# Optimization experiments

Hardware: AMD Instinct MI355X
Metric: run time of the kernel (lower is better)

Reference implementation:

```python
import jax, jax.numpy as jnp
import numpy as np

N = 300000
H = 700
W_GRID = 700
CIN = 64
COUT = 64
K = 9


def setup_inputs() -> dict:
    rng = np.random.default_rng(0)
    lin = rng.permutation(H * W_GRID)[:N]
    ys = (lin // W_GRID).astype(np.int64)
    xs = (lin % W_GRID).astype(np.int64)
    grid = np.full(H * W_GRID, -1, np.int32)
    grid[lin] = np.arange(N, dtype=np.int32)
    offs = [(dy, dx) for dy in (-1, 0, 1) for dx in (-1, 0, 1)]

    def build(d):
        nbr = np.full((K, N), -1, np.int32)
        for k, (dy, dx) in enumerate(offs):
            ny = ys + dy * d
            nx = xs + dx * d
            valid = (ny >= 0) & (ny < H) & (nx >= 0) & (nx < W_GRID)
            l = np.clip(ny * W_GRID + nx, 0, H * W_GRID - 1)
            nbr[k] = np.where(valid, grid[l], -1)
        return jnp.asarray(nbr)

    nbr_d1 = build(1)
    nbr_d2 = build(2)

    key = jax.random.key(0)
    ks = jax.random.split(key, 16)
    f32 = jnp.float32

    def bn(k, c):
        s = jax.random.uniform(k, (c,), f32, 0.5, 1.5)
        b = jax.random.normal(jax.random.fold_in(k, 1), (c,), f32) * 0.1
        return s, b

    features = jax.random.normal(ks[0], (N, CIN), f32)
    W1 = jax.random.normal(ks[1], (K, CIN, COUT), f32) * 0.05
    W2a = jax.random.normal(ks[2], (CIN, COUT // 2), f32) * 0.05
    W2b = jax.random.normal(ks[3], (K, COUT // 2, COUT), f32) * 0.05
    W3 = jax.random.normal(ks[4], (K, CIN, COUT), f32) * 0.05
    Wf = jax.random.normal(ks[5], (3 * COUT, COUT), f32) * 0.05
    A1_w = jax.random.normal(ks[6], (3 * COUT, COUT // 4), f32) * 0.1
    A1_b = jnp.zeros((COUT // 4,), f32)
    A2_w = jax.random.normal(ks[7], (COUT // 4, 3 * COUT), f32) * 0.1
    A2_b = jnp.zeros((3 * COUT,), f32)
    bn1_s, bn1_b = bn(ks[8], COUT)
    bn2a_s, bn2a_b = bn(ks[9], COUT // 2)
    bn2b_s, bn2b_b = bn(ks[10], COUT)
    bn3_s, bn3_b = bn(ks[11], COUT)
    bnf_s, bnf_b = bn(ks[12], COUT)

    return dict(features=features, W1=W1, bn1_s=bn1_s, bn1_b=bn1_b,
                W2a=W2a, bn2a_s=bn2a_s, bn2a_b=bn2a_b,
                W2b=W2b, bn2b_s=bn2b_s, bn2b_b=bn2b_b,
                W3=W3, bn3_s=bn3_s, bn3_b=bn3_b,
                A1_w=A1_w, A1_b=A1_b, A2_w=A2_w, A2_b=A2_b,
                Wf=Wf, bnf_s=bnf_s, bnf_b=bnf_b,
                nbr_d1=nbr_d1, nbr_d2=nbr_d2)


def _sconv(f, nbr, W):
    # f: [N, Cin], nbr: [K, N] (-1 = no neighbor), W: [K, Cin, Cout]
    mask = (nbr >= 0)[..., None]                      # [K, N, 1]
    g = jnp.where(mask, f[jnp.clip(nbr, 0)], 0.0)     # [K, N, Cin] gather
    return jnp.einsum('knc,kcd->nd', g, W)            # [N, Cout]


def _bnrelu(x, s, b):
    # inference-mode BatchNorm folded into affine scale/shift, then ReLU
    return jax.nn.relu(x * s + b)


def reference(features, W1, bn1_s, bn1_b, W2a, bn2a_s, bn2a_b, W2b, bn2b_s, bn2b_b,
              W3, bn3_s, bn3_b, A1_w, A1_b, A2_w, A2_b, Wf, bnf_s, bnf_b,
              nbr_d1, nbr_d2):
    # path 1: 3x3 sparse conv + BN + ReLU
    feat1 = _bnrelu(_sconv(features, nbr_d1, W1), bn1_s, bn1_b)
    # path 2: 1x1 bottleneck + 3x3 sparse conv
    h = _bnrelu(features @ W2a, bn2a_s, bn2a_b)
    feat2 = _bnrelu(_sconv(h, nbr_d1, W2b), bn2b_s, bn2b_b)
    # path 3: 3x3 dilated (d=2) sparse conv
    feat3 = _bnrelu(_sconv(features, nbr_d2, W3), bn3_s, bn3_b)
    ms = jnp.concatenate([feat1, feat2, feat3], axis=1)   # [N, 3*Cout]
    # SE-style attention from global max pool over active sites
    pooled = jnp.max(ms, axis=0)                          # [3*Cout]
    attn = jax.nn.sigmoid(jax.nn.relu(pooled @ A1_w + A1_b) @ A2_w + A2_b)
    ms = ms * attn
    # 1x1 fusion conv + BN + ReLU
    fused = _bnrelu(ms @ Wf, bnf_s, bnf_b)                # [N, Cout]
    return fused
```

## Files before the change

kernel.cpp:

```cpp
#include <hip/hip_runtime.h>

#define N_PTS 300000
#define NPAD  300032
#define ZROW  N_PTS

typedef _Float16 f16;
typedef _Float16 f16x8 __attribute__((ext_vector_type(8)));
typedef float    f32x4 __attribute__((ext_vector_type(4)));

__device__ __forceinline__ f16 f2h(float x) { return (f16)x; }

union u4f16 { uint4 u; f16x8 h; };

#define HEAD_BLOCKS (NPAD / 256)
#define WP_BLOCKS   361


__global__ __launch_bounds__(256) void k_head(
    const float* __restrict__ feat, const float* __restrict__ W2a,
    const float* __restrict__ s2a, const float* __restrict__ b2a,
    const float* __restrict__ W1, const float* __restrict__ W2b,
    const float* __restrict__ W3,
    f16* __restrict__ featf, f16* __restrict__ hf,
    f16* __restrict__ Wt1, f16* __restrict__ Wt2b, f16* __restrict__ Wt3,
    float* __restrict__ pooled)
{
    if (blockIdx.x >= HEAD_BLOCKS) {
        int i = (blockIdx.x - HEAD_BLOCKS) * 256 + threadIdx.x;
        if (i < 36864) {
            int j = i & 7, lane = (i >> 3) & 63, nt = (i >> 9) & 3,
                ks = (i >> 11) & 1, k = i >> 12;
            int d = ks * 32 + (lane >> 4) * 8 + j, c = nt * 16 + (lane & 15);
            Wt1[i] = f2h(W1[(k << 12) + (d << 6) + c]);
        } else if (i < 73728) {
            int ii = i - 36864;
            int j = ii & 7, lane = (ii >> 3) & 63, nt = (ii >> 9) & 3,
                ks = (ii >> 11) & 1, k = ii >> 12;
            int d = ks * 32 + (lane >> 4) * 8 + j, c = nt * 16 + (lane & 15);
            Wt3[ii] = f2h(W3[(k << 12) + (d << 6) + c]);
        } else if (i < 92160) {
            int ii = i - 73728;
            int j = ii & 7, lane = (ii >> 3) & 63, nt = (ii >> 9) & 3, k = ii >> 11;
            int d = (lane >> 4) * 8 + j, c = nt * 16 + (lane & 15);
            Wt2b[ii] = f2h(W2b[k * 2048 + (d << 6) + c]);
        } else if (i < 92352) {
            pooled[i - 92160] = 0.f;
        }
        return;
    }

    int lane = threadIdx.x & 63, wave = threadIdx.x >> 6;
    int n0 = (blockIdx.x * 4 + wave) * 64;
    int ln = lane & 15, q = lane >> 4;

    f16x8 a[4][2];
#pragma unroll
    for (int mt = 0; mt < 4; mt++) {
        int n = n0 + mt * 16 + ln;
#pragma unroll
        for (int ks = 0; ks < 2; ks++) {
            u4f16 v;
            if (n < N_PTS) {
                const float* p = feat + (long)n * 64 + ks * 32 + q * 8;
                float4 lo = *(const float4*)p;
                float4 hi = *(const float4*)(p + 4);
                v.h[0] = f2h(lo.x); v.h[1] = f2h(lo.y);
                v.h[2] = f2h(lo.z); v.h[3] = f2h(lo.w);
                v.h[4] = f2h(hi.x); v.h[5] = f2h(hi.y);
                v.h[6] = f2h(hi.z); v.h[7] = f2h(hi.w);
            } else {
                v.u = make_uint4(0u, 0u, 0u, 0u);
            }
            a[mt][ks] = v.h;
            *(uint4*)(featf + (long)n * 64 + ks * 32 + q * 8) = v.u;
        }
    }

    f32x4 acc[4][2];
    for (int mt = 0; mt < 4; mt++) for (int nt = 0; nt < 2; nt++)
        acc[mt][nt] = (f32x4){0.f, 0.f, 0.f, 0.f};
#pragma unroll
    for (int ks = 0; ks < 2; ks++)
#pragma unroll
        for (int nt = 0; nt < 2; nt++) {
            f16x8 b;
#pragma unroll
            for (int j = 0; j < 8; j++)
                b[j] = f2h(W2a[(ks * 32 + q * 8 + j) * 32 + nt * 16 + ln]);
#pragma unroll
            for (int mt = 0; mt < 4; mt++)
                acc[mt][nt] = __builtin_amdgcn_mfma_f32_16x16x32_f16(a[mt][ks], b, acc[mt][nt], 0, 0, 0);
        }

#pragma unroll
    for (int nt = 0; nt < 2; nt++) {
        int ch = nt * 16 + ln;
        float s = s2a[ch], bb = b2a[ch];
#pragma unroll
        for (int mt = 0; mt < 4; mt++)
#pragma unroll
            for (int r = 0; r < 4; r++) {
                int n = n0 + mt * 16 + q * 4 + r;
                float v = (n < N_PTS) ? fmaxf(acc[mt][nt][r] * s + bb, 0.f) : 0.f;
                hf[(long)n * 32 + ch] = f2h(v);
            }
    }
}

template <int CIN>
__device__ __forceinline__ void loadrows(
    uint4 (&dst)[4][CIN / 32], const int (&idx)[4],
    const f16* __restrict__ src, int q)
{
#pragma unroll
    for (int mt = 0; mt < 4; mt++) {
        const f16* p = src + (long)idx[mt] * CIN + q * 8;
#pragma unroll
        for (int ks = 0; ks < CIN / 32; ks++)
            dst[mt][ks] = *(const uint4*)(p + ks * 32);
    }
}

__device__ __forceinline__ void loadidx(
    int (&dst)[4], const int* __restrict__ nbr, int k, int n0, int ln)
{
    const int* nb = nbr + k * N_PTS;
#pragma unroll
    for (int mt = 0; mt < 4; mt++) {
        int nn = n0 + mt * 16 + ln;
        int v = (nn < N_PTS) ? nb[nn] : -1;
        dst[mt] = (v < 0) ? ZROW : v;
    }
}

template <int CIN>
__device__ __forceinline__ void conv_path(
    const f16* __restrict__ src, const f16* WtL,
    const int* __restrict__ nbr,
    int lane, int n0,
    const float* __restrict__ bns, const float* __restrict__ bnb,
    f16* __restrict__ msf, int colBase, float* __restrict__ pooled)
{
    constexpr int KS = CIN / 32;
    int ln = lane & 15, q = lane >> 4;

    f32x4 acc[4][4];
    for (int mt = 0; mt < 4; mt++) for (int nt = 0; nt < 4; nt++)
        acc[mt][nt] = (f32x4){0.f, 0.f, 0.f, 0.f};

    int  idxr[4][4];
    uint4 raw[4][4][KS];

#pragma unroll
    for (int k = 0; k < 4; k++) loadidx(idxr[k], nbr, k, n0, ln);
#pragma unroll
    for (int k = 0; k < 3; k++) loadrows<CIN>(raw[k], idxr[k], src, q);
    __builtin_amdgcn_sched_barrier(0);

#pragma unroll
    for (int k = 0; k < 9; k++) {
        if (k + 3 < 9) loadrows<CIN>(raw[(k + 3) & 3], idxr[(k + 3) & 3], src, q);
        if (k + 4 < 9) loadidx(idxr[k & 3], nbr, k + 4, n0, ln);
        __builtin_amdgcn_sched_barrier(0);
        const f16* Wk = WtL + k * (KS * 4 * 512);
        __builtin_amdgcn_s_setprio(1);
#pragma unroll
        for (int ks = 0; ks < KS; ks++)
#pragma unroll
            for (int nt = 0; nt < 4; nt++) {
                f16x8 b = *(const f16x8*)(Wk + (ks * 4 + nt) * 512 + lane * 8);
#pragma unroll
                for (int mt = 0; mt < 4; mt++) {
                    u4f16 v; v.u = raw[k & 3][mt][ks];
                    acc[mt][nt] = __builtin_amdgcn_mfma_f32_16x16x32_f16(v.h, b, acc[mt][nt], 0, 0, 0);
                }
            }
        __builtin_amdgcn_s_setprio(0);
    }

#pragma unroll
    for (int nt = 0; nt < 4; nt++) {
        int ch = colBase + nt * 16 + ln;
        float s = bns[nt * 16 + ln], bb = bnb[nt * 16 + ln];
        float cmax = 0.f;
#pragma unroll
        for (int mt = 0; mt < 4; mt++)
#pragma unroll
            for (int r = 0; r < 4; r++) {
                int n = n0 + mt * 16 + q * 4 + r;
                float v = fmaxf(acc[mt][nt][r] * s + bb, 0.f);
                msf[(long)n * 192 + ch] = f2h(v);
                if (n < N_PTS) cmax = fmaxf(cmax, v);
            }
        cmax = fmaxf(cmax, __shfl_xor(cmax, 16));
        cmax = fmaxf(cmax, __shfl_xor(cmax, 32));
        if (q == 0) atomicMax((int*)(pooled + ch), __float_as_int(cmax));
    }
}

__global__ __launch_bounds__(512, 2) void k_conv(
    const f16* __restrict__ featf, const f16* __restrict__ hf,
    const f16* __restrict__ Wt1, const f16* __restrict__ Wt2b, const f16* __restrict__ Wt3,
    const int* __restrict__ nbr1, const int* __restrict__ nbr2,
    const float* __restrict__ bn1_s, const float* __restrict__ bn1_b,
    const float* __restrict__ bn2b_s, const float* __restrict__ bn2b_b,
    const float* __restrict__ bn3_s, const float* __restrict__ bn3_b,
    f16* __restrict__ msf, float* __restrict__ pooled)
{
    __shared__ f16 smem[9 * 64 * 64];

    int path = blockIdx.x % 3;
    int g    = blockIdx.x / 3;
    int lane = threadIdx.x & 63, wave = threadIdx.x >> 6;
    int n0 = (g * 8 + wave) * 64;

    const f16* Wsrc = (path == 0) ? Wt1 : (path == 1) ? Wt2b : Wt3;
    int nchunk = (path == 1) ? (9 * 32 * 64 / 8) : (9 * 64 * 64 / 8);
    for (int i = threadIdx.x; i < nchunk; i += 512)
        ((uint4*)smem)[i] = ((const uint4*)Wsrc)[i];
    __syncthreads();

    if (path == 0)
        conv_path<64>(featf, smem, nbr1, lane, n0, bn1_s,  bn1_b,  msf, 0,   pooled);
    else if (path == 1)
        conv_path<32>(hf,    smem, nbr1, lane, n0, bn2b_s, bn2b_b, msf, 64,  pooled);
    else
        conv_path<64>(featf, smem, nbr2, lane, n0, bn3_s,  bn3_b,  msf, 128, pooled);
}

__global__ __launch_bounds__(256, 4) void k_fuse(
    const f16* __restrict__ msf, const float* __restrict__ pooled,
    const float* __restrict__ A1w, const float* __restrict__ A1b,
    const float* __restrict__ A2w, const float* __restrict__ A2b,
    const float* __restrict__ Wf,
    const float* __restrict__ sf, const float* __restrict__ bf_,
    float* __restrict__ out)
{
    __shared__ float sp[192], sa1[16], sattn[192];
    __shared__ f16 sWf[12288];
    int t = threadIdx.x;
    if (t < 192) sp[t] = pooled[t];
    __syncthreads();
    if (t < 16) {
        float a = A1b[t];
        for (int i = 0; i < 192; i++) a += sp[i] * A1w[i * 16 + t];
        sa1[t] = fmaxf(a, 0.f);
    }
    __syncthreads();
    if (t < 192) {
        float a = A2b[t];
        for (int i = 0; i < 16; i++) a += sa1[i] * A2w[i * 192 + t];
        sattn[t] = 1.f / (1.f + expf(-a));
    }
    __syncthreads();
    for (int i = t; i < 12288; i += 256) {
        int j = i & 7, lane = (i >> 3) & 63, nt = (i >> 9) & 3, kt = i >> 11;
        int jrow = kt * 32 + (lane >> 4) * 8 + j, c = nt * 16 + (lane & 15);
        sWf[i] = f2h(Wf[jrow * 64 + c] * sattn[jrow]);
    }
    __syncthreads();

    int lane = threadIdx.x & 63, wave = threadIdx.x >> 6;
    int n0 = (blockIdx.x * 4 + wave) * 32;
    int ln = lane & 15, q = lane >> 4;

    uint4 araw[6][2];
#pragma unroll
    for (int kt = 0; kt < 6; kt++)
#pragma unroll
        for (int mt = 0; mt < 2; mt++)
            araw[kt][mt] = *(const uint4*)(msf + (long)(n0 + mt * 16 + ln) * 192 + kt * 32 + q * 8);

    f32x4 acc[2][4];
    for (int mt = 0; mt < 2; mt++) for (int nt = 0; nt < 4; nt++)
        acc[mt][nt] = (f32x4){0.f, 0.f, 0.f, 0.f};

#pragma unroll
    for (int kt = 0; kt < 6; kt++)
#pragma unroll
        for (int nt = 0; nt < 4; nt++) {
            f16x8 b = *(const f16x8*)(sWf + ((kt * 4 + nt) * 64 + lane) * 8);
#pragma unroll
            for (int mt = 0; mt < 2; mt++) {
                u4f16 v; v.u = araw[kt][mt];
                acc[mt][nt] = __builtin_amdgcn_mfma_f32_16x16x32_f16(v.h, b, acc[mt][nt], 0, 0, 0);
            }
        }

#pragma unroll
    for (int nt = 0; nt < 4; nt++) {
        int ch = nt * 16 + ln;
        float s = sf[ch], bb = bf_[ch];
#pragma unroll
        for (int mt = 0; mt < 2; mt++)
#pragma unroll
            for (int r = 0; r < 4; r++) {
                int n = n0 + mt * 16 + q * 4 + r;
                if (n < N_PTS)
                    __builtin_nontemporal_store(fmaxf(acc[mt][nt][r] * s + bb, 0.f),
                                                &out[(long)n * 64 + ch]);
            }
    }
}

extern "C" void kernel_launch(void* const* d_in, const int* in_sizes, int n_in,
                              void* d_out, int out_size, void* d_ws, size_t ws_size,
                              hipStream_t stream)
{
    const float* features = (const float*)d_in[0];
    const float* W1     = (const float*)d_in[1];
    const float* bn1_s  = (const float*)d_in[2];
    const float* bn1_b  = (const float*)d_in[3];
    const float* W2a    = (const float*)d_in[4];
    const float* bn2a_s = (const float*)d_in[5];
    const float* bn2a_b = (const float*)d_in[6];
    const float* W2b    = (const float*)d_in[7];
    const float* bn2b_s = (const float*)d_in[8];
    const float* bn2b_b = (const float*)d_in[9];
    const float* W3     = (const float*)d_in[10];
    const float* bn3_s  = (const float*)d_in[11];
    const float* bn3_b  = (const float*)d_in[12];
    const float* A1w    = (const float*)d_in[13];
    const float* A1b    = (const float*)d_in[14];
    const float* A2w    = (const float*)d_in[15];
    const float* A2b    = (const float*)d_in[16];
    const float* Wf     = (const float*)d_in[17];
    const float* bnf_s  = (const float*)d_in[18];
    const float* bnf_b  = (const float*)d_in[19];
    const int*   nbr1   = (const int*)d_in[20];
    const int*   nbr2   = (const int*)d_in[21];

    char* ws = (char*)d_ws;
    size_t off = 0;
    f16* featf = (f16*)(ws + off); off += (size_t)NPAD * 64 * 2;
    f16* hf    = (f16*)(ws + off); off += (size_t)NPAD * 32 * 2;
    f16* msf   = (f16*)(ws + off); off += (size_t)NPAD * 192 * 2;
    f16* Wt1   = (f16*)(ws + off); off += 9 * 64 * 64 * 2;
    f16* Wt3   = (f16*)(ws + off); off += 9 * 64 * 64 * 2;
    f16* Wt2b  = (f16*)(ws + off); off += 9 * 32 * 64 * 2;
    float* pooled = (float*)(ws + off); off += 256 * 4;

    k_head<<<HEAD_BLOCKS + WP_BLOCKS, 256, 0, stream>>>(
        features, W2a, bn2a_s, bn2a_b, W1, W2b, W3,
        featf, hf, Wt1, Wt2b, Wt3, pooled);

    k_conv<<<(NPAD / 64 / 8) * 3, 512, 0, stream>>>(featf, hf, Wt1, Wt2b, Wt3, nbr1, nbr2,
                                           bn1_s, bn1_b, bn2b_s, bn2b_b, bn3_s, bn3_b,
                                           msf, pooled);

    k_fuse<<<NPAD / 128, 256, 0, stream>>>(msf, pooled, A1w, A1b, A2w, A2b, Wf,
                                           bnf_s, bnf_b, (float*)d_out);
}
```

Before: 416.7 us.

## Merge three kernels into one persistent cooperative kernel with grid syncs

```diff
diff --git a/kernel.cpp b/kernel.cpp
--- a/kernel.cpp
+++ b/kernel.cpp
@@ -1,4 +1,7 @@
 #include <hip/hip_runtime.h>
+#include <hip/hip_cooperative_groups.h>
+
+namespace cg = cooperative_groups;
 
 #define N_PTS 300000
 #define NPAD  300032
@@ -12,45 +15,42 @@
 
 union u4f16 { uint4 u; f16x8 h; };
 
-#define HEAD_BLOCKS (NPAD / 256)
-#define WP_BLOCKS   361
-
-
-__global__ __launch_bounds__(256) void k_head(
-    const float* __restrict__ feat, const float* __restrict__ W2a,
-    const float* __restrict__ s2a, const float* __restrict__ b2a,
-    const float* __restrict__ W1, const float* __restrict__ W2b,
-    const float* __restrict__ W3,
-    f16* __restrict__ featf, f16* __restrict__ hf,
-    f16* __restrict__ Wt1, f16* __restrict__ Wt2b, f16* __restrict__ Wt3,
-    float* __restrict__ pooled)
-{
-    if (blockIdx.x >= HEAD_BLOCKS) {
-        int i = (blockIdx.x - HEAD_BLOCKS) * 256 + threadIdx.x;
-        if (i < 36864) {
-            int j = i & 7, lane = (i >> 3) & 63, nt = (i >> 9) & 3,
-                ks = (i >> 11) & 1, k = i >> 12;
-            int d = ks * 32 + (lane >> 4) * 8 + j, c = nt * 16 + (lane & 15);
-            Wt1[i] = f2h(W1[(k << 12) + (d << 6) + c]);
-        } else if (i < 73728) {
-            int ii = i - 36864;
-            int j = ii & 7, lane = (ii >> 3) & 63, nt = (ii >> 9) & 3,
-                ks = (ii >> 11) & 1, k = ii >> 12;
-            int d = ks * 32 + (lane >> 4) * 8 + j, c = nt * 16 + (lane & 15);
-            Wt3[ii] = f2h(W3[(k << 12) + (d << 6) + c]);
-        } else if (i < 92160) {
-            int ii = i - 73728;
-            int j = ii & 7, lane = (ii >> 3) & 63, nt = (ii >> 9) & 3, k = ii >> 11;
-            int d = (lane >> 4) * 8 + j, c = nt * 16 + (lane & 15);
-            Wt2b[ii] = f2h(W2b[k * 2048 + (d << 6) + c]);
-        } else if (i < 92352) {
-            pooled[i - 92160] = 0.f;
-        }
-        return;
-    }
-
-    int lane = threadIdx.x & 63, wave = threadIdx.x >> 6;
-    int n0 = (blockIdx.x * 4 + wave) * 64;
+
+struct Params {
+    const float *feat, *W2a, *s2a, *b2a, *W1, *W2b, *W3;
+    const float *A1w, *A1b, *A2w, *A2b, *Wf, *sf, *bf;
+    const float *bn1_s, *bn1_b, *bn2b_s, *bn2b_b, *bn3_s, *bn3_b;
+    const int *nbr1, *nbr2;
+    f16 *featf, *hf, *msf, *Wt1, *Wt2b, *Wt3;
+    float *pooled, *out;
+};
+
+__device__ __forceinline__ void repack_elem(const Params& P, int i)
+{
+    if (i < 36864) {
+        int j = i & 7, lane = (i >> 3) & 63, nt = (i >> 9) & 3,
+            ks = (i >> 11) & 1, k = i >> 12;
+        int d = ks * 32 + (lane >> 4) * 8 + j, c = nt * 16 + (lane & 15);
+        P.Wt1[i] = f2h(P.W1[(k << 12) + (d << 6) + c]);
+    } else if (i < 73728) {
+        int ii = i - 36864;
+        int j = ii & 7, lane = (ii >> 3) & 63, nt = (ii >> 9) & 3,
+            ks = (ii >> 11) & 1, k = ii >> 12;
+        int d = ks * 32 + (lane >> 4) * 8 + j, c = nt * 16 + (lane & 15);
+        P.Wt3[ii] = f2h(P.W3[(k << 12) + (d << 6) + c]);
+    } else if (i < 92160) {
+        int ii = i - 73728;
+        int j = ii & 7, lane = (ii >> 3) & 63, nt = (ii >> 9) & 3, k = ii >> 11;
+        int d = (lane >> 4) * 8 + j, c = nt * 16 + (lane & 15);
+        P.Wt2b[ii] = f2h(P.W2b[k * 2048 + (d << 6) + c]);
+    } else if (i < 92352) {
+        P.pooled[i - 92160] = 0.f;
+    }
+}
+
+__device__ __forceinline__ void head_unit(const Params& P, int u, int lane)
+{
+    int n0 = u * 64;
     int ln = lane & 15, q = lane >> 4;
 
     f16x8 a[4][2];
@@ -61,7 +61,7 @@
         for (int ks = 0; ks < 2; ks++) {
             u4f16 v;
             if (n < N_PTS) {
-                const float* p = feat + (long)n * 64 + ks * 32 + q * 8;
+                const float* p = P.feat + (long)n * 64 + ks * 32 + q * 8;
                 float4 lo = *(const float4*)p;
                 float4 hi = *(const float4*)(p + 4);
                 v.h[0] = f2h(lo.x); v.h[1] = f2h(lo.y);
@@ -72,7 +72,7 @@
                 v.u = make_uint4(0u, 0u, 0u, 0u);
             }
             a[mt][ks] = v.h;
-            *(uint4*)(featf + (long)n * 64 + ks * 32 + q * 8) = v.u;
+            *(uint4*)(P.featf + (long)n * 64 + ks * 32 + q * 8) = v.u;
         }
     }
 
@@ -86,7 +86,7 @@
             f16x8 b;
 #pragma unroll
             for (int j = 0; j < 8; j++)
-                b[j] = f2h(W2a[(ks * 32 + q * 8 + j) * 32 + nt * 16 + ln]);
+                b[j] = f2h(P.W2a[(ks * 32 + q * 8 + j) * 32 + nt * 16 + ln]);
 #pragma unroll
             for (int mt = 0; mt < 4; mt++)
                 acc[mt][nt] = __builtin_amdgcn_mfma_f32_16x16x32_f16(a[mt][ks], b, acc[mt][nt], 0, 0, 0);
@@ -95,14 +95,14 @@
 #pragma unroll
     for (int nt = 0; nt < 2; nt++) {
         int ch = nt * 16 + ln;
-        float s = s2a[ch], bb = b2a[ch];
+        float s = P.s2a[ch], bb = P.b2a[ch];
 #pragma unroll
         for (int mt = 0; mt < 4; mt++)
 #pragma unroll
             for (int r = 0; r < 4; r++) {
                 int n = n0 + mt * 16 + q * 4 + r;
                 float v = (n < N_PTS) ? fmaxf(acc[mt][nt][r] * s + bb, 0.f) : 0.f;
-                hf[(long)n * 32 + ch] = f2h(v);
+                P.hf[(long)n * 32 + ch] = f2h(v);
             }
     }
 }
@@ -198,70 +198,10 @@
     }
 }
 
-__global__ __launch_bounds__(512, 2) void k_conv(
-    const f16* __restrict__ featf, const f16* __restrict__ hf,
-    const f16* __restrict__ Wt1, const f16* __restrict__ Wt2b, const f16* __restrict__ Wt3,
-    const int* __restrict__ nbr1, const int* __restrict__ nbr2,
-    const float* __restrict__ bn1_s, const float* __restrict__ bn1_b,
-    const float* __restrict__ bn2b_s, const float* __restrict__ bn2b_b,
-    const float* __restrict__ bn3_s, const float* __restrict__ bn3_b,
-    f16* __restrict__ msf, float* __restrict__ pooled)
-{
-    __shared__ f16 smem[9 * 64 * 64];
-
-    int path = blockIdx.x % 3;
-    int g    = blockIdx.x / 3;
-    int lane = threadIdx.x & 63, wave = threadIdx.x >> 6;
-    int n0 = (g * 8 + wave) * 64;
-
-    const f16* Wsrc = (path == 0) ? Wt1 : (path == 1) ? Wt2b : Wt3;
-    int nchunk = (path == 1) ? (9 * 32 * 64 / 8) : (9 * 64 * 64 / 8);
-    for (int i = threadIdx.x; i < nchunk; i += 512)
-        ((uint4*)smem)[i] = ((const uint4*)Wsrc)[i];
-    __syncthreads();
-
-    if (path == 0)
-        conv_path<64>(featf, smem, nbr1, lane, n0, bn1_s,  bn1_b,  msf, 0,   pooled);
-    else if (path == 1)
-        conv_path<32>(hf,    smem, nbr1, lane, n0, bn2b_s, bn2b_b, msf, 64,  pooled);
-    else
-        conv_path<64>(featf, smem, nbr2, lane, n0, bn3_s,  bn3_b,  msf, 128, pooled);
-}
-
-__global__ __launch_bounds__(256, 4) void k_fuse(
-    const f16* __restrict__ msf, const float* __restrict__ pooled,
-    const float* __restrict__ A1w, const float* __restrict__ A1b,
-    const float* __restrict__ A2w, const float* __restrict__ A2b,
-    const float* __restrict__ Wf,
-    const float* __restrict__ sf, const float* __restrict__ bf_,
-    float* __restrict__ out)
-{
-    __shared__ float sp[192], sa1[16], sattn[192];
-    __shared__ f16 sWf[12288];
-    int t = threadIdx.x;
-    if (t < 192) sp[t] = pooled[t];
-    __syncthreads();
-    if (t < 16) {
-        float a = A1b[t];
-        for (int i = 0; i < 192; i++) a += sp[i] * A1w[i * 16 + t];
-        sa1[t] = fmaxf(a, 0.f);
-    }
-    __syncthreads();
-    if (t < 192) {
-        float a = A2b[t];
-        for (int i = 0; i < 16; i++) a += sa1[i] * A2w[i * 192 + t];
-        sattn[t] = 1.f / (1.f + expf(-a));
-    }
-    __syncthreads();
-    for (int i = t; i < 12288; i += 256) {
-        int j = i & 7, lane = (i >> 3) & 63, nt = (i >> 9) & 3, kt = i >> 11;
-        int jrow = kt * 32 + (lane >> 4) * 8 + j, c = nt * 16 + (lane & 15);
-        sWf[i] = f2h(Wf[jrow * 64 + c] * sattn[jrow]);
-    }
-    __syncthreads();
-
-    int lane = threadIdx.x & 63, wave = threadIdx.x >> 6;
-    int n0 = (blockIdx.x * 4 + wave) * 32;
+__device__ __forceinline__ void fuse_unit(
+    const Params& P, const f16* sWf, int g, int wave, int lane)
+{
+    int n0 = g * 256 + wave * 32;
     int ln = lane & 15, q = lane >> 4;
 
     uint4 araw[6][2];
@@ -269,7 +209,7 @@
     for (int kt = 0; kt < 6; kt++)
 #pragma unroll
         for (int mt = 0; mt < 2; mt++)
-            araw[kt][mt] = *(const uint4*)(msf + (long)(n0 + mt * 16 + ln) * 192 + kt * 32 + q * 8);
+            araw[kt][mt] = *(const uint4*)(P.msf + (long)(n0 + mt * 16 + ln) * 192 + kt * 32 + q * 8);
 
     f32x4 acc[2][4];
     for (int mt = 0; mt < 2; mt++) for (int nt = 0; nt < 4; nt++)
@@ -290,7 +230,7 @@
 #pragma unroll
     for (int nt = 0; nt < 4; nt++) {
         int ch = nt * 16 + ln;
-        float s = sf[ch], bb = bf_[ch];
+        float s = P.sf[ch], bb = P.bf[ch];
 #pragma unroll
         for (int mt = 0; mt < 2; mt++)
 #pragma unroll
@@ -298,8 +238,74 @@
                 int n = n0 + mt * 16 + q * 4 + r;
                 if (n < N_PTS)
                     __builtin_nontemporal_store(fmaxf(acc[mt][nt][r] * s + bb, 0.f),
-                                                &out[(long)n * 64 + ch]);
-            }
+                                                &P.out[(long)n * 64 + ch]);
+            }
+    }
+}
+
+__global__ __launch_bounds__(512, 4) void k_mega(Params P, int phases)
+{
+    __shared__ __align__(16) char smemraw[9 * 64 * 64 * 2];
+
+    int tid = threadIdx.x, lane = tid & 63, wave = tid >> 6;
+    int G = gridDim.x;
+
+    if (phases & 1) {
+        for (int i = blockIdx.x * 512 + tid; i < 92352; i += G * 512)
+            repack_elem(P, i);
+        for (int u = blockIdx.x * 8 + wave; u < 4688; u += G * 8)
+            head_unit(P, u, lane);
+    }
+    if (phases == 7) { __threadfence(); cg::this_grid().sync(); }
+
+    if (phases & 2) {
+        int path = blockIdx.x % 3, b3 = blockIdx.x / 3, NB3 = G / 3;
+        f16* smem = (f16*)smemraw;
+        const f16* Wsrc = (path == 0) ? P.Wt1 : (path == 1) ? P.Wt2b : P.Wt3;
+        int nchunk = (path == 1) ? (9 * 32 * 64 / 8) : (9 * 64 * 64 / 8);
+        for (int i = tid; i < nchunk; i += 512)
+            ((uint4*)smemraw)[i] = ((const uint4*)Wsrc)[i];
+        __syncthreads();
+        for (int g = b3; g < 586; g += NB3) {
+            int n0 = (g * 8 + wave) * 64;
+            if (path == 0)
+                conv_path<64>(P.featf, smem, P.nbr1, lane, n0, P.bn1_s,  P.bn1_b,  P.msf, 0,   P.pooled);
+            else if (path == 1)
+                conv_path<32>(P.hf,    smem, P.nbr1, lane, n0, P.bn2b_s, P.bn2b_b, P.msf, 64,  P.pooled);
+            else
+                conv_path<64>(P.featf, smem, P.nbr2, lane, n0, P.bn3_s,  P.bn3_b,  P.msf, 128, P.pooled);
+        }
+    }
+    if (phases == 7) { __threadfence(); cg::this_grid().sync(); }
+
+    if (phases & 4) {
+        float* sp    = (float*)smemraw;
+        float* sa1   = (float*)(smemraw + 768);
+        float* sattn = (float*)(smemraw + 832);
+        f16*   sWf   = (f16*)(smemraw + 1600);
+        __syncthreads();
+        if (tid < 192) sp[tid] = P.pooled[tid];
+        __syncthreads();
+        if (tid < 16) {
+            float a = P.A1b[tid];
+            for (int i = 0; i < 192; i++) a += sp[i] * P.A1w[i * 16 + tid];
+            sa1[tid] = fmaxf(a, 0.f);
+        }
+        __syncthreads();
+        if (tid < 192) {
+            float a = P.A2b[tid];
+            for (int i = 0; i < 16; i++) a += sa1[i] * P.A2w[i * 192 + tid];
+            sattn[tid] = 1.f / (1.f + expf(-a));
+        }
+        __syncthreads();
+        for (int i = tid; i < 12288; i += 512) {
+            int j = i & 7, ll = (i >> 3) & 63, nt = (i >> 9) & 3, kt = i >> 11;
+            int jrow = kt * 32 + (ll >> 4) * 8 + j, c = nt * 16 + (ll & 15);
+            sWf[i] = f2h(P.Wf[jrow * 64 + c] * sattn[jrow]);
+        }
+        __syncthreads();
+        for (int g = blockIdx.x; g < 1172; g += G)
+            fuse_unit(P, sWf, g, wave, lane);
     }
 }
 
@@ -307,29 +313,6 @@
                               void* d_out, int out_size, void* d_ws, size_t ws_size,
                               hipStream_t stream)
 {
-    const float* features = (const float*)d_in[0];
-    const float* W1     = (const float*)d_in[1];
-    const float* bn1_s  = (const float*)d_in[2];
-    const float* bn1_b  = (const float*)d_in[3];
-    const float* W2a    = (const float*)d_in[4];
-    const float* bn2a_s = (const float*)d_in[5];
-    const float* bn2a_b = (const float*)d_in[6];
-    const float* W2b    = (const float*)d_in[7];
-    const float* bn2b_s = (const float*)d_in[8];
-    const float* bn2b_b = (const float*)d_in[9];
-    const float* W3     = (const float*)d_in[10];
-    const float* bn3_s  = (const float*)d_in[11];
-    const float* bn3_b  = (const float*)d_in[12];
-    const float* A1w    = (const float*)d_in[13];
-    const float* A1b    = (const float*)d_in[14];
-    const float* A2w    = (const float*)d_in[15];
-    const float* A2b    = (const float*)d_in[16];
-    const float* Wf     = (const float*)d_in[17];
-    const float* bnf_s  = (const float*)d_in[18];
-    const float* bnf_b  = (const float*)d_in[19];
-    const int*   nbr1   = (const int*)d_in[20];
-    const int*   nbr2   = (const int*)d_in[21];
-
     char* ws = (char*)d_ws;
     size_t off = 0;
     f16* featf = (f16*)(ws + off); off += (size_t)NPAD * 64 * 2;
@@ -340,14 +323,59 @@
     f16* Wt2b  = (f16*)(ws + off); off += 9 * 32 * 64 * 2;
     float* pooled = (float*)(ws + off); off += 256 * 4;
 
-    k_head<<<HEAD_BLOCKS + WP_BLOCKS, 256, 0, stream>>>(
-        features, W2a, bn2a_s, bn2a_b, W1, W2b, W3,
-        featf, hf, Wt1, Wt2b, Wt3, pooled);
-
-    k_conv<<<(NPAD / 64 / 8) * 3, 512, 0, stream>>>(featf, hf, Wt1, Wt2b, Wt3, nbr1, nbr2,
-                                           bn1_s, bn1_b, bn2b_s, bn2b_b, bn3_s, bn3_b,
-                                           msf, pooled);
-
-    k_fuse<<<NPAD / 128, 256, 0, stream>>>(msf, pooled, A1w, A1b, A2w, A2b, Wf,
-                                           bnf_s, bnf_b, (float*)d_out);
-}
+    Params P;
+    P.feat   = (const float*)d_in[0];
+    P.W1     = (const float*)d_in[1];
+    P.bn1_s  = (const float*)d_in[2];
+    P.bn1_b  = (const float*)d_in[3];
+    P.W2a    = (const float*)d_in[4];
+    P.s2a    = (const float*)d_in[5];
+    P.b2a    = (const float*)d_in[6];
+    P.W2b    = (const float*)d_in[7];
+    P.bn2b_s = (const float*)d_in[8];
+    P.bn2b_b = (const float*)d_in[9];
+    P.W3     = (const float*)d_in[10];
+    P.bn3_s  = (const float*)d_in[11];
+    P.bn3_b  = (const float*)d_in[12];
+    P.A1w    = (const float*)d_in[13];
+    P.A1b    = (const float*)d_in[14];
+    P.A2w    = (const float*)d_in[15];
+    P.A2b    = (const float*)d_in[16];
+    P.Wf     = (const float*)d_in[17];
+    P.sf     = (const float*)d_in[18];
+    P.bf     = (const float*)d_in[19];
+    P.nbr1   = (const int*)d_in[20];
+    P.nbr2   = (const int*)d_in[21];
+    P.featf = featf; P.hf = hf; P.msf = msf;
+    P.Wt1 = Wt1; P.Wt2b = Wt2b; P.Wt3 = Wt3;
+    P.pooled = pooled; P.out = (float*)d_out;
+
+    static int s_init = 0, s_coop = 0, s_G = 255;
+    if (!s_init) {
+        int coop = 0, ncu = 0, occ = 0;
+        if (hipDeviceGetAttribute(&coop, hipDeviceAttributeCooperativeLaunch, 0) != hipSuccess) coop = 0;
+        if (hipDeviceGetAttribute(&ncu, hipDeviceAttributeMultiprocessorCount, 0) != hipSuccess || ncu <= 0) ncu = 256;
+        if (hipOccupancyMaxActiveBlocksPerMultiprocessor(
+                &occ, reinterpret_cast<const void*>(k_mega), 512, 0) != hipSuccess || occ <= 0) occ = 1;
+        s_coop = coop;
+        s_G = (occ * ncu / 3) * 3;
+        if (s_G < 3) s_G = 3;
+        s_init = 1;
+    }
+
+    if (s_coop) {
+        int phases = 7;
+        void* args[] = { (void*)&P, (void*)&phases };
+        if (hipLaunchCooperativeKernel(reinterpret_cast<const void*>(k_mega),
+                                       dim3(s_G), dim3(512), args, 0u, stream) != hipSuccess) {
+            s_coop = 0;
+            k_mega<<<s_G, 512, 0, stream>>>(P, 1);
+            k_mega<<<s_G, 512, 0, stream>>>(P, 2);
+            k_mega<<<s_G, 512, 0, stream>>>(P, 4);
+        }
+    } else {
+        k_mega<<<s_G, 512, 0, stream>>>(P, 1);
+        k_mega<<<s_G, 512, 0, stream>>>(P, 2);
+        k_mega<<<s_G, 512, 0, stream>>>(P, 4);
+    }
+}
```

New measurement: 978.1 us. 135% more time.
